# Optimization experiments

Hardware: AMD Instinct MI355X
Metric: run time of the kernel (lower is better)

The kernel has to match this reference:

```python
import jax, jax.numpy as jnp
import numpy as np

N, E, D, F, L = 50000, 250000, 128, 12, 4
EPS_POS = 1e-6
EPS_LN = 1e-5


def setup_inputs() -> dict:
    key = jax.random.key(0)
    ks = iter(jax.random.split(key, 40))
    w = lambda *s: jax.random.normal(next(ks), s, dtype=jnp.float32) * 0.05
    inp = {
        'node_features': jax.random.normal(next(ks), (N, F), dtype=jnp.float32),
        'pos': jax.random.normal(next(ks), (N, 2), dtype=jnp.float32),
        'edge_attr_raw': jax.random.normal(next(ks), (E, F), dtype=jnp.float32),
        'node_proj_w': w(F, D), 'node_proj_b': jnp.zeros((D,), jnp.float32),
        'edge_proj_w': w(F, D), 'edge_proj_b': jnp.zeros((D,), jnp.float32),
        'edge_w1': w(L, 2 * D + 1, D), 'edge_b1': jnp.zeros((L, D), jnp.float32),
        'edge_w2': w(L, D, D), 'edge_b2': jnp.zeros((L, D), jnp.float32),
        'node_w1': w(L, 2 * D, D), 'node_b1': jnp.zeros((L, D), jnp.float32),
        'node_w2': w(L, D, D), 'node_b2': jnp.zeros((L, D), jnp.float32),
        'pos_w1': w(L, D + 1, 1), 'pos_b1': jnp.zeros((L, 1), jnp.float32),
        'pos_w2': w(L, 1, 1), 'pos_b2': jnp.zeros((L, 1), jnp.float32),
        'ln_g': jnp.ones((D,), jnp.float32), 'ln_b': jnp.zeros((D,), jnp.float32),
        'edge_index': jax.random.randint(next(ks), (2, E), 0, N, dtype=jnp.int32),
    }
    return inp


def reference(node_features, pos, edge_attr_raw,
              node_proj_w, node_proj_b, edge_proj_w, edge_proj_b,
              edge_w1, edge_b1, edge_w2, edge_b2,
              node_w1, node_b1, node_w2, node_b2,
              pos_w1, pos_b1, pos_w2, pos_b2,
              ln_g, ln_b, edge_index):
    src, tgt = edge_index[0], edge_index[1]
    n = node_features.shape[0]
    x = node_features @ node_proj_w + node_proj_b          # [N, D]
    # edge_projection output is concatenated then sliced away in the original
    # (edge_input[:, :2D+1]); it is mathematically dead but computed faithfully.
    _edge_attr = edge_attr_raw @ edge_proj_w + edge_proj_b  # dead
    p = pos                                                  # [N, 2]
    for l in range(L):
        xs, xt = x[src], x[tgt]                              # [E, D]
        ps, pt = p[src], p[tgt]                              # [E, 2]
        dist = jnp.linalg.norm(ps - pt, axis=1, keepdims=True)  # [E, 1]
        e_in = jnp.concatenate([xs, xt, dist], axis=1)       # [E, 2D+1]
        msg = jax.nn.silu(e_in @ edge_w1[l] + edge_b1[l]) @ edge_w2[l] + edge_b2[l]
        pos_diff = pt - ps
        pos_unit = pos_diff / (jnp.linalg.norm(pos_diff, axis=1, keepdims=True) + EPS_POS)
        pw = jax.nn.silu(jnp.concatenate([msg, dist], axis=1) @ pos_w1[l] + pos_b1[l])
        pw = pw @ pos_w2[l] + pos_b2[l]                       # [E, 1]
        p = p + jax.ops.segment_sum(pos_unit * pw, tgt, num_segments=n)
        agg = jax.ops.segment_sum(msg, tgt, num_segments=n)  # [N, D]
        n_in = jnp.concatenate([x, agg], axis=1)              # [N, 2D]
        x = x + (jax.nn.silu(n_in @ node_w1[l] + node_b1[l]) @ node_w2[l] + node_b2[l])
    mu = jnp.mean(x, axis=-1, keepdims=True)
    var = jnp.mean(jnp.square(x - mu), axis=-1, keepdims=True)
    x = (x - mu) * jax.lax.rsqrt(var + EPS_LN) * ln_g + ln_b
    return x[None]                                            # [1, N, D]
```

## Files before the change

### kernel.cpp

```cpp
#include <hip/hip_runtime.h>
#include <hip/hip_bf16.h>


#define NNODES 50000
#define NEDGES 250000
#define NTILES 3125
#define MMGRID 512
#define RGRID  1024

typedef unsigned short u16;
typedef __attribute__((ext_vector_type(8))) short bf16x8;
typedef __attribute__((ext_vector_type(4))) float floatx4;

__device__ __forceinline__ float b2f(u16 h){ unsigned u=((unsigned)h)<<16; float f; __builtin_memcpy(&f,&u,4); return f; }
__device__ __forceinline__ u16 f2b(float f){ unsigned u; __builtin_memcpy(&u,&f,4); u = u + 0x7FFFu + ((u>>16)&1u); return (u16)(u>>16); }
__device__ __forceinline__ float siluf(float x){ return x*__builtin_amdgcn_rcpf(1.f+__expf(-x)); }
__device__ __forceinline__ float ldf(const void* p, long i, int isbf){
  return isbf ? b2f(((const u16*)p)[i]) : ((const float*)p)[i];
}

__global__ void detect_kernel(const void* lng, int* flag){
  if (threadIdx.x==0 && blockIdx.x==0) *flag = (((const u16*)lng)[0] != 0) ? 1 : 0;
}

#define SU_W12   192
#define SU_EBW   704
#define SU_W2P   708
#define SU_PPARM 712
#define SU_PROJ  713
#define SU_CVTP  25713
#define SU_END   26104
__global__ __launch_bounds__(256) void setup_kernel(
    const void* __restrict__ ew1, const void* __restrict__ ew2,
    const void* __restrict__ nw1, const void* __restrict__ nw2,
    u16* __restrict__ packed,
    const void* __restrict__ eb2, const void* __restrict__ pw1,
    const void* __restrict__ pb1, const void* __restrict__ pw2v, const void* __restrict__ pb2,
    float* __restrict__ w2p, float* __restrict__ c2p, float* __restrict__ pparm,
    float* __restrict__ ebW,
    const void* __restrict__ nf, const void* __restrict__ npw, const void* __restrict__ npb,
    u16* __restrict__ xb,
    const void* __restrict__ pos, float* __restrict__ pf,
    const int* __restrict__ flagp)
{
  const int isbf = *flagp;
  const int b = blockIdx.x, tid = threadIdx.x;
  __shared__ float red[128];
  if (b < SU_W12){
    int t = b*256 + tid;
    int m = t >> 11; int r = t & 2047;
    int lane = r & 63; int ntk = r >> 6;
    int kk = ntk >> 3, nt = ntk & 7;
    int l = m/6, w = m%6;
    const void* src; long off;
    switch(w){
      case 0: src=ew1; off=(long)l*257*128;            break;
      case 1: src=ew1; off=(long)l*257*128 + 128*128;  break;
      case 2: src=ew2; off=(long)l*128*128;            break;
      case 3: src=nw1; off=(long)l*256*128;            break;
      case 4: src=nw1; off=(long)l*256*128 + 128*128;  break;
      default:src=nw2; off=(long)l*128*128;            break;
    }
    int c  = nt*16 + (lane & 15);
    int k0 = kk*32 + (lane >> 4)*8;
    u16 vals[8];
#pragma unroll
    for (int j=0;j<8;j++){
      long idx = off + (long)(k0+j)*128 + c;
      vals[j] = isbf ? ((const u16*)src)[idx] : f2b(((const float*)src)[idx]);
    }
    bf16x8 v; __builtin_memcpy(&v, vals, 16);
    *(bf16x8*)(packed + (long)t*8) = v;
  } else if (b < SU_EBW){
    int bb = b - SU_W12;
    int l = bb >> 7, k = bb & 127;
    if (tid < 128){
      int j = tid;
      long e2 = (long)l*16384 + (long)k*128;
      long nb = (long)l*256*128 + 128*128;
      float acc = 0.f;
      for (int d=0; d<128; d++)
        acc += ldf(ew2, e2 + d, isbf) * ldf(nw1, nb + (long)d*128 + j, isbf);
      int kk = k>>5, lane = ((k>>3)&3)*16 + (j&15), nt = j>>4, jj = k&7;
      packed[(long)(24+l)*16384 + (long)((kk*8+nt)*64 + lane)*8 + jj] = f2b(acc);
    }
  } else if (b < SU_W2P){
    int l = b - SU_EBW;
    if (tid < 128){
      int j = tid;
      long nb = (long)l*256*128 + 128*128;
      float acc = 0.f;
      for (int d=0; d<128; d++)
        acc += ldf(eb2, (long)l*128 + d, isbf) * ldf(nw1, nb + (long)d*128 + j, isbf);
      ebW[l*128+j] = acc;
    }
  } else if (b < SU_PPARM){
    int l = b - SU_W2P;
    int i = tid;
    long Woff = (long)l*128*128, poff = (long)l*129;
    if (i < 128){
      float acc = 0.f;
      for (int j=0;j<128;j++) acc += ldf(ew2, Woff + (long)i*128 + j, isbf) * ldf(pw1, poff + j, isbf);
      w2p[l*128+i] = acc;
      red[i] = ldf(eb2, (long)l*128 + i, isbf) * ldf(pw1, poff + i, isbf);
    }
    __syncthreads();
    for (int st=64; st>0; st>>=1){ if (i<st) red[i]+=red[i+st]; __syncthreads(); }
    if (i==0) c2p[l] = red[0];
  } else if (b == SU_PPARM){
    int l = tid;
    if (l < 4){
      pparm[l*4+0] = ldf(pw1, (long)l*129 + 128, isbf);
      pparm[l*4+1] = ldf(pb1, l, isbf);
      pparm[l*4+2] = ldf(pw2v, l, isbf);
      pparm[l*4+3] = ldf(pb2, l, isbf);
    }
  } else if (b < SU_CVTP){
    int n = (b - SU_PROJ)*2 + (tid>>7), d = tid & 127;
    if (n < NNODES){
      float acc = ldf(npb, d, isbf);
#pragma unroll
      for (int f=0; f<12; f++) acc += ldf(nf, (long)n*12+f, isbf) * ldf(npw, f*128+d, isbf);
      xb[(long)n*128+d] = f2b(acc);
    }
  } else {
    int i = (b - SU_CVTP)*256 + tid;
    if (i < 2*NNODES) pf[i] = ldf(pos, i, isbf);
  }
}

__global__ __launch_bounds__(256) void hist_kernel(const int* __restrict__ tgt, int* __restrict__ cnt, int E){
  int i = blockIdx.x*256 + threadIdx.x;
  if (i < E) atomicAdd(&cnt[tgt[i]], 1);
}

__global__ __launch_bounds__(256) void bsum_kernel(const int* __restrict__ cnt, int* __restrict__ bsum, int N){
  int i = blockIdx.x*256 + threadIdx.x;
  int v = (i < N) ? cnt[i] : 0;
#pragma unroll
  for (int off=32; off; off>>=1) v += __shfl_down(v, off);
  __shared__ int ws[4];
  if ((threadIdx.x & 63) == 0) ws[threadIdx.x>>6] = v;
  __syncthreads();
  if (threadIdx.x == 0) bsum[blockIdx.x] = ws[0]+ws[1]+ws[2]+ws[3];
}

__global__ __launch_bounds__(256) void bscan_kernel(int* __restrict__ bsum, int nb){
  __shared__ int lds[256];
  int i = threadIdx.x;
  int v = (i < nb) ? bsum[i] : 0;
  lds[i] = v; __syncthreads();
#pragma unroll
  for (int off=1; off<256; off<<=1){
    int t = (i>=off)? lds[i-off] : 0; __syncthreads();
    lds[i] += t; __syncthreads();
  }
  if (i < nb) bsum[i] = lds[i] - v;
}

__global__ __launch_bounds__(256) void csr_kernel(
    const int* __restrict__ cnt, const int* __restrict__ bsum,
    int* __restrict__ rowptr, int* __restrict__ cursor, float* __restrict__ degf, int N)
{
  __shared__ int lds[256];
  int i = blockIdx.x*256 + threadIdx.x;
  int c = (i < N) ? cnt[i] : 0;
  lds[threadIdx.x] = c; __syncthreads();
#pragma unroll
  for (int off=1; off<256; off<<=1){
    int t = (threadIdx.x>=off)? lds[threadIdx.x-off] : 0; __syncthreads();
    lds[threadIdx.x] += t; __syncthreads();
  }
  int run = bsum[blockIdx.x] + lds[threadIdx.x] - c;
  if (i < N){
    rowptr[i] = run; cursor[i] = run; degf[i] = (float)c;
    if (i == N-1) rowptr[N] = run + c;
  }
}

__global__ __launch_bounds__(256) void scatter_kernel(
    const int* __restrict__ src, const int* __restrict__ tgt,
    int* __restrict__ cursor, int* __restrict__ permsrc, int E)
{
  int e = blockIdx.x*256 + threadIdx.x;
  if (e >= E) return;
  int t = tgt[e];
  int p = atomicAdd(&cursor[t], 1);
  permsrc[p] = src[e];
}

__global__ __launch_bounds__(256) void mm_ab_kernel(
    const u16* __restrict__ X, const u16* __restrict__ Wa, const u16* __restrict__ Wb,
    const void* __restrict__ bias, long bias_off,
    u16* __restrict__ Ab, u16* __restrict__ Bb, const int* __restrict__ flagp)
{
  extern __shared__ u16 wlds[];
  const int tid = threadIdx.x, wave = tid>>6, lane = tid&63;
  const int isbf = *flagp;
  const int lr = lane&15, lg = lane>>4;
  for (int i=tid; i<2048; i+=256){
    *(bf16x8*)(wlds + (long)i*8)          = *(const bf16x8*)(Wa + (long)i*8);
    *(bf16x8*)(wlds + 16384 + (long)i*8)  = *(const bf16x8*)(Wb + (long)i*8);
  }
  float biasv[8];
#pragma unroll
  for (int nt=0;nt<8;nt++) biasv[nt] = ldf(bias, bias_off + nt*16 + lr, isbf);
  __syncthreads();
  for (int tile = blockIdx.x*4 + wave; tile < NTILES; tile += MMGRID*4){
    const u16* xr = X + ((long)tile*16 + lr)*128;
    bf16x8 a[4];
#pragma unroll
    for (int kk=0;kk<4;kk++) a[kk] = *(const bf16x8*)(xr + kk*32 + lg*8);
    floatx4 accA[8], accB[8];
#pragma unroll
    for (int i=0;i<8;i++){ accA[i]=(floatx4){0,0,0,0}; accB[i]=(floatx4){0,0,0,0}; }
#pragma unroll
    for (int kk=0;kk<4;kk++){
#pragma unroll
      for (int nt=0;nt<8;nt++){
        bf16x8 ba = *(const bf16x8*)(wlds + ((kk*8+nt)*64 + lane)*8);
        accA[nt] = __builtin_amdgcn_mfma_f32_16x16x32_bf16(a[kk], ba, accA[nt], 0, 0, 0);
        bf16x8 bb = *(const bf16x8*)(wlds + 16384 + ((kk*8+nt)*64 + lane)*8);
        accB[nt] = __builtin_amdgcn_mfma_f32_16x16x32_bf16(a[kk], bb, accB[nt], 0, 0, 0);
      }
    }
#pragma unroll
    for (int r=0;r<4;r++){
      long row = (long)tile*16 + lg*4 + r;
#pragma unroll
      for (int nt=0;nt<8;nt++){
        int col = nt*16 + lr;
        Ab[row*128+col] = f2b(accA[nt][r] + biasv[nt]);
        Bb[row*128+col] = f2b(accB[nt][r]);
      }
    }
  }
}

__global__ __launch_bounds__(256) void mm_hidden_kernel(
    const u16* __restrict__ X, const u16* __restrict__ H,
    const u16* __restrict__ W1, const u16* __restrict__ W2,
    const void* __restrict__ nb1, long nb1_off,
    const float* __restrict__ degf, const float* __restrict__ ebW,
    u16* __restrict__ hb, const int* __restrict__ flagp)
{
  extern __shared__ u16 wlds[];
  const int tid = threadIdx.x, wave = tid>>6, lane = tid&63;
  const int isbf = *flagp;
  const int lr = lane&15, lg = lane>>4;
  for (int i=tid; i<2048; i+=256){
    *(bf16x8*)(wlds + (long)i*8)          = *(const bf16x8*)(W1 + (long)i*8);
    *(bf16x8*)(wlds + 16384 + (long)i*8)  = *(const bf16x8*)(W2 + (long)i*8);
  }
  float nb1v[8], ebv[8];
#pragma unroll
  for (int nt=0;nt<8;nt++){ int col=nt*16+lr; nb1v[nt]=ldf(nb1, nb1_off+col, isbf); ebv[nt]=ebW[col]; }
  __syncthreads();
  for (int tile = blockIdx.x*4 + wave; tile < NTILES; tile += MMGRID*4){
    const u16* xr = X + ((long)tile*16 + lr)*128;
    const u16* hr = H + ((long)tile*16 + lr)*128;
    bf16x8 ax[4], ah[4];
#pragma unroll
    for (int kk=0;kk<4;kk++){
      ax[kk] = *(const bf16x8*)(xr + kk*32 + lg*8);
      ah[kk] = *(const bf16x8*)(hr + kk*32 + lg*8);
    }
    floatx4 acc[8];
#pragma unroll
    for (int i=0;i<8;i++) acc[i]=(floatx4){0,0,0,0};
#pragma unroll
    for (int kk=0;kk<4;kk++){
#pragma unroll
      for (int nt=0;nt<8;nt++){
        bf16x8 b1 = *(const bf16x8*)(wlds + ((kk*8+nt)*64 + lane)*8);
        acc[nt] = __builtin_amdgcn_mfma_f32_16x16x32_bf16(ax[kk], b1, acc[nt], 0, 0, 0);
        bf16x8 b2 = *(const bf16x8*)(wlds + 16384 + ((kk*8+nt)*64 + lane)*8);
        acc[nt] = __builtin_amdgcn_mfma_f32_16x16x32_bf16(ah[kk], b2, acc[nt], 0, 0, 0);
      }
    }
    float dv[4];
#pragma unroll
    for (int r=0;r<4;r++) dv[r] = degf[(long)tile*16 + lg*4 + r];
#pragma unroll
    for (int r=0;r<4;r++){
      long row = (long)tile*16 + lg*4 + r;
#pragma unroll
      for (int nt=0;nt<8;nt++){
        int col = nt*16 + lr;
        hb[row*128+col] = f2b(siluf(acc[nt][r] + nb1v[nt] + dv[r]*ebv[nt]));
      }
    }
  }
}

template<int LN>
__global__ __launch_bounds__(256) void mm_res_kernel(
    const u16* __restrict__ H, const u16* __restrict__ W,
    const void* __restrict__ nb2, long nb2_off,
    u16* __restrict__ xb,
    const void* __restrict__ lng, const void* __restrict__ lnb, void* __restrict__ outp,
    const int* __restrict__ flagp)
{
  extern __shared__ u16 wlds[];
  const int tid = threadIdx.x, wave = tid>>6, lane = tid&63;
  const int isbf = *flagp;
  const int lr = lane&15, lg = lane>>4;
  for (int i=tid; i<2048; i+=256)
    *(bf16x8*)(wlds + (long)i*8) = *(const bf16x8*)(W + (long)i*8);
  float nb2v[8];
#pragma unroll
  for (int nt=0;nt<8;nt++) nb2v[nt] = ldf(nb2, nb2_off + nt*16 + lr, isbf);
  float gv[8], bvv[8];
  if (LN){
#pragma unroll
    for (int nt=0;nt<8;nt++){ int col=nt*16+lr; gv[nt]=ldf(lng,col,isbf); bvv[nt]=ldf(lnb,col,isbf); }
  }
  __syncthreads();
  for (int tile = blockIdx.x*4 + wave; tile < NTILES; tile += RGRID*4){
    const u16* hr = H + ((long)tile*16 + lr)*128;
    bf16x8 a[4];
#pragma unroll
    for (int kk=0;kk<4;kk++) a[kk] = *(const bf16x8*)(hr + kk*32 + lg*8);
    floatx4 acc[8];
#pragma unroll
    for (int i=0;i<8;i++) acc[i]=(floatx4){0,0,0,0};
#pragma unroll
    for (int kk=0;kk<4;kk++){
#pragma unroll
      for (int nt=0;nt<8;nt++){
        bf16x8 b = *(const bf16x8*)(wlds + ((kk*8+nt)*64 + lane)*8);
        acc[nt] = __builtin_amdgcn_mfma_f32_16x16x32_bf16(a[kk], b, acc[nt], 0, 0, 0);
      }
    }
#pragma unroll
    for (int r=0;r<4;r++){
      long row = (long)tile*16 + lg*4 + r;
#pragma unroll
      for (int nt=0;nt<8;nt++){
        int col = nt*16 + lr;
        float v = acc[nt][r] + nb2v[nt] + b2f(xb[row*128+col]);
        acc[nt][r] = v;
        if (!LN) xb[row*128+col] = f2b(v);
      }
    }
    if (LN){
      float s[4] = {0,0,0,0}, q[4] = {0,0,0,0};
#pragma unroll
      for (int r=0;r<4;r++){
#pragma unroll
        for (int nt=0;nt<8;nt++){ float v = acc[nt][r]; s[r] += v; q[r] += v*v; }
      }
#pragma unroll
      for (int mask=1; mask<16; mask<<=1){
#pragma unroll
        for (int r=0;r<4;r++){ s[r] += __shfl_xor(s[r], mask); q[r] += __shfl_xor(q[r], mask); }
      }
#pragma unroll
      for (int r=0;r<4;r++){
        long row = (long)tile*16 + lg*4 + r;
        float mu = s[r]*(1.f/128.f);
        float var = q[r]*(1.f/128.f) - mu*mu;
        float inv = rsqrtf(var + 1e-5f);
#pragma unroll
        for (int nt=0;nt<8;nt++){
          int col = nt*16 + lr;
          float y = (acc[nt][r]-mu)*inv*gv[nt] + bvv[nt];
          if (isbf) ((u16*)outp)[row*128+col] = f2b(y);
          else      ((float*)outp)[row*128+col] = y;
        }
      }
    }
  }
}

__global__ __launch_bounds__(256) void agg_kernel(
    const int* __restrict__ rowptr, const int* __restrict__ permsrc,
    const float* __restrict__ pf_in,
    const u16* __restrict__ A, const u16* __restrict__ B,
    const void* __restrict__ ew1, long w1c_off,
    const float* __restrict__ w2p, const float* __restrict__ c2pl,
    const float* __restrict__ pp,
    u16* __restrict__ Hb, float* __restrict__ pf_out, int N,
    const int* __restrict__ flagp)
{
  const int isbf = *flagp;
  int tid = threadIdx.x, lane = tid & 63;
  int t = blockIdx.x*4 + (tid>>6);
  if (t >= N) return;
  int tu = __builtin_amdgcn_readfirstlane(t);
  float c0 = ldf(ew1, w1c_off + 2*lane,     isbf);
  float c1 = ldf(ew1, w1c_off + 2*lane + 1, isbf);
  float2 wp = *(const float2*)(w2p + 2*lane);
  float c2 = c2pl[0];
  float p0 = pp[0], p1 = pp[1], p2 = pp[2], p3 = pp[3];
  int jb = rowptr[tu], je = rowptr[tu+1];
  float2 pt = *(const float2*)(pf_in + 2*(long)tu);
  unsigned bv = *(const unsigned*)(B + (long)tu*128 + 2*lane);
  float b0 = b2f((u16)bv), b1 = b2f((u16)(bv>>16));
  float h0a = 0.f, h1a = 0.f, dpx = 0.f, dpy = 0.f;
  for (int j0 = jb; j0 < je; j0 += 4){
    int m = je - j0; if (m > 4) m = 4;
    int s[4]; float2 ps[4]; unsigned av[4];
    float part[4], dist[4], dxv[4], dyv[4];
#pragma unroll
    for (int c=0;c<4;c++) if (c<m) s[c] = permsrc[j0+c];
#pragma unroll
    for (int c=0;c<4;c++) if (c<m){
      ps[c] = *(const float2*)(pf_in + 2*(long)s[c]);
      av[c] = *(const unsigned*)(A + (long)s[c]*128 + 2*lane);
    }
#pragma unroll
    for (int c=0;c<4;c++){
      if (c<m){
        float dx = pt.x - ps[c].x, dy = pt.y - ps[c].y;
        float d2 = dx*dx + dy*dy;
        float dd = __builtin_amdgcn_sqrtf(d2);
        float h0 = siluf(b2f((u16)av[c])       + b0 + dd*c0);
        float h1 = siluf(b2f((u16)(av[c]>>16)) + b1 + dd*c1);
        h0a += h0; h1a += h1;
        part[c] = h0*wp.x + h1*wp.y;
        dist[c] = dd; dxv[c] = dx; dyv[c] = dy;
      } else part[c] = 0.f;
    }
#pragma unroll
    for (int off=32; off; off>>=1){
#pragma unroll
      for (int c=0;c<4;c++) part[c] += __shfl_xor(part[c], off);
    }
#pragma unroll
    for (int c=0;c<4;c++){
      if (c<m){
        float spre = part[c] + c2 + dist[c]*p0 + p1;
        float pwv  = siluf(spre)*p2 + p3;
        float inv  = __builtin_amdgcn_rcpf(dist[c] + 1e-6f);
        dpx += dxv[c]*inv*pwv; dpy += dyv[c]*inv*pwv;
      }
    }
  }
  *(unsigned*)(Hb + (long)tu*128 + 2*lane) = (unsigned)f2b(h0a) | ((unsigned)f2b(h1a)<<16);
  if (lane == 0){
    float2 o; o.x = pt.x + dpx; o.y = pt.y + dpy;
    *(float2*)(pf_out + 2*(long)tu) = o;
  }
}

extern "C" void kernel_launch(void* const* d_in, const int* in_sizes, int n_in,
                              void* d_out, int out_size, void* d_ws, size_t ws_size,
                              hipStream_t stream)
{
  const void* nf  = d_in[0];
  const void* pos = d_in[1];
  const void* npw = d_in[3];
  const void* npb = d_in[4];
  const void* ew1 = d_in[7];
  const void* eb1 = d_in[8];
  const void* ew2 = d_in[9];
  const void* eb2 = d_in[10];
  const void* nw1 = d_in[11];
  const void* nb1 = d_in[12];
  const void* nw2 = d_in[13];
  const void* nb2 = d_in[14];
  const void* pw1 = d_in[15];
  const void* pb1 = d_in[16];
  const void* pw2 = d_in[17];
  const void* pb2 = d_in[18];
  const void* lng = d_in[19];
  const void* lnb = d_in[20];
  const int* eidx = (const int*)d_in[21];
  const int N = NNODES, E = NEDGES;
  const int* srcp = eidx;
  const int* tgtp = eidx + E;

  char* w = (char*)d_ws;
  size_t off = 0;
  auto alloc = [&](size_t bytes)->char* { char* p = w + off; off += (bytes + 255)/256*256; return p; };
  u16*   xb    = (u16*)  alloc((size_t)N*128*2);
  u16*   Ab    = (u16*)  alloc((size_t)N*128*2);
  u16*   Bb    = (u16*)  alloc((size_t)N*128*2);
  u16*   Hb    = (u16*)  alloc((size_t)N*128*2);
  float* pf0   = (float*)alloc((size_t)N*2*4);
  float* pf1   = (float*)alloc((size_t)N*2*4);
  int*   cnt   = (int*)  alloc((size_t)N*4);
  int*   rowptr= (int*)  alloc((size_t)(N+1)*4);
  int*   cursor= (int*)  alloc((size_t)N*4);
  float* degf  = (float*)alloc((size_t)N*4);
  int*   perm  = (int*)  alloc((size_t)E*4);
  int*   bsum  = (int*)  alloc(256*4);
  u16*   pk    = (u16*)  alloc((size_t)28*16384*2);
  float* ebW   = (float*)alloc(4*128*4);
  float* w2p   = (float*)alloc(4*128*4);
  float* c2p   = (float*)alloc(4*4);
  float* pparm = (float*)alloc(16*4);
  int*   flag  = (int*)  alloc(4);
  u16* hb = Ab;

  const int NB = (N + 255)/256;
  detect_kernel<<<1, 64, 0, stream>>>(lng, flag);
  hipMemsetAsync(cnt, 0, (size_t)N*4, stream);
  hist_kernel<<<(E+255)/256, 256, 0, stream>>>(tgtp, cnt, E);
  bsum_kernel<<<NB, 256, 0, stream>>>(cnt, bsum, N);
  bscan_kernel<<<1, 256, 0, stream>>>(bsum, NB);
  csr_kernel<<<NB, 256, 0, stream>>>(cnt, bsum, rowptr, cursor, degf, N);
  scatter_kernel<<<(E+255)/256, 256, 0, stream>>>(srcp, tgtp, cursor, perm, E);
  setup_kernel<<<SU_END, 256, 0, stream>>>(
      ew1, ew2, nw1, nw2, pk,
      eb2, pw1, pb1, pw2, pb2,
      w2p, c2p, pparm, ebW,
      nf, npw, npb, xb,
      pos, pf0, flag);

  mm_ab_kernel<<<MMGRID, 256, 65536, stream>>>(xb, pk + 0*16384, pk + 1*16384,
                                               eb1, 0, Ab, Bb, flag);
  for (int l = 0; l < 4; l++){
    const u16* NW1a = pk + (l*6+3)*16384;
    const u16* NW2p = pk + (l*6+5)*16384;
    const u16* W12p = pk + (24+l)*16384;
    float* pin  = (l & 1) ? pf1 : pf0;
    float* pout = (l & 1) ? pf0 : pf1;

    agg_kernel<<<(N+3)/4, 256, 0, stream>>>(
        rowptr, perm, pin, Ab, Bb,
        ew1, (long)l*257*128 + 256*128,
        w2p + l*128, c2p + l, pparm + l*4,
        Hb, pout, N, flag);
    mm_hidden_kernel<<<MMGRID, 256, 65536, stream>>>(
        xb, Hb, NW1a, W12p, nb1, (long)l*128, degf, ebW + l*128, hb, flag);
    if (l < 3){
      mm_res_kernel<0><<<RGRID, 256, 32768, stream>>>(
          hb, NW2p, nb2, (long)l*128, xb, nullptr, nullptr, nullptr, flag);
      mm_ab_kernel<<<MMGRID, 256, 65536, stream>>>(
          xb, pk + ((l+1)*6+0)*16384, pk + ((l+1)*6+1)*16384,
          eb1, (long)(l+1)*128, Ab, Bb, flag);
    } else {
      mm_res_kernel<1><<<RGRID, 256, 32768, stream>>>(
          hb, NW2p, nb2, (long)l*128, xb, lng, lnb, d_out, flag);
    }
  }
}
```

Measured before the change: 524.4 us.

## Merge setup and CSR-build kernels into one cooperative grid-synced kernel

Replaces the detect, memset, histogram, block-sum, scan, CSR, scatter and setup kernels with a single cooperative kernel. It runs these as phases separated by grid.sync and interleaves independent weight-packing work into the phases. The aim is to remove several launch gaps and small-kernel tails. In exchange it adds grid-wide barriers, and a 512-block grid must stride over large phases such as the 25000-block node projection, which may run with lower parallelism than before.

```diff
diff --git a/kernel.cpp b/kernel.cpp
--- a/kernel.cpp
+++ b/kernel.cpp
@@ -1,5 +1,8 @@
 #include <hip/hip_runtime.h>
 #include <hip/hip_bf16.h>
+#include <hip/hip_cooperative_groups.h>
+
+namespace cg = cooperative_groups;
 
 
 #define NNODES 50000
@@ -7,6 +10,7 @@
 #define NTILES 3125
 #define MMGRID 512
 #define RGRID  1024
+#define COOPGRID 512
 
 typedef unsigned short u16;
 typedef __attribute__((ext_vector_type(8))) short bf16x8;
@@ -19,18 +23,22 @@
   return isbf ? b2f(((const u16*)p)[i]) : ((const float*)p)[i];
 }
 
-__global__ void detect_kernel(const void* lng, int* flag){
-  if (threadIdx.x==0 && blockIdx.x==0) *flag = (((const u16*)lng)[0] != 0) ? 1 : 0;
-}
-
-#define SU_W12   192
-#define SU_EBW   704
-#define SU_W2P   708
-#define SU_PPARM 712
-#define SU_PROJ  713
-#define SU_CVTP  25713
-#define SU_END   26104
-__global__ __launch_bounds__(256) void setup_kernel(
+#define P0_MEMSET 196
+#define P0_CVTP   587
+#define P0_END    596
+#define P1_HIST   977
+#define P1_END    1169
+#define P2_BSUM   196
+#define P2_END    708
+#define P3_END    25001
+#define P4_END    196
+#define P5_END    977
+
+__global__ __launch_bounds__(256, 4) void coop_setup_kernel(
+    const void* __restrict__ lng, int* __restrict__ flag,
+    const int* __restrict__ src, const int* __restrict__ tgt,
+    int* __restrict__ cnt, int* __restrict__ bsum, int* __restrict__ rowptr,
+    int* __restrict__ cursor, float* __restrict__ degf, int* __restrict__ permsrc,
     const void* __restrict__ ew1, const void* __restrict__ ew2,
     const void* __restrict__ nw1, const void* __restrict__ nw2,
     u16* __restrict__ packed,
@@ -40,153 +48,169 @@
     float* __restrict__ ebW,
     const void* __restrict__ nf, const void* __restrict__ npw, const void* __restrict__ npb,
     u16* __restrict__ xb,
-    const void* __restrict__ pos, float* __restrict__ pf,
-    const int* __restrict__ flagp)
+    const void* __restrict__ pos, float* __restrict__ pf)
 {
-  const int isbf = *flagp;
-  const int b = blockIdx.x, tid = threadIdx.x;
+  cg::grid_group grid = cg::this_grid();
+  const int tid = threadIdx.x;
+  const int isbf = (((const u16*)lng)[0] != 0) ? 1 : 0;
+  __shared__ int slds[256];
   __shared__ float red[128];
-  if (b < SU_W12){
-    int t = b*256 + tid;
-    int m = t >> 11; int r = t & 2047;
-    int lane = r & 63; int ntk = r >> 6;
-    int kk = ntk >> 3, nt = ntk & 7;
-    int l = m/6, w = m%6;
-    const void* src; long off;
-    switch(w){
-      case 0: src=ew1; off=(long)l*257*128;            break;
-      case 1: src=ew1; off=(long)l*257*128 + 128*128;  break;
-      case 2: src=ew2; off=(long)l*128*128;            break;
-      case 3: src=nw1; off=(long)l*256*128;            break;
-      case 4: src=nw1; off=(long)l*256*128 + 128*128;  break;
-      default:src=nw2; off=(long)l*128*128;            break;
-    }
-    int c  = nt*16 + (lane & 15);
-    int k0 = kk*32 + (lane >> 4)*8;
-    u16 vals[8];
-#pragma unroll
-    for (int j=0;j<8;j++){
-      long idx = off + (long)(k0+j)*128 + c;
-      vals[j] = isbf ? ((const u16*)src)[idx] : f2b(((const float*)src)[idx]);
-    }
-    bf16x8 v; __builtin_memcpy(&v, vals, 16);
-    *(bf16x8*)(packed + (long)t*8) = v;
-  } else if (b < SU_EBW){
-    int bb = b - SU_W12;
-    int l = bb >> 7, k = bb & 127;
-    if (tid < 128){
-      int j = tid;
-      long e2 = (long)l*16384 + (long)k*128;
-      long nb = (long)l*256*128 + 128*128;
-      float acc = 0.f;
-      for (int d=0; d<128; d++)
-        acc += ldf(ew2, e2 + d, isbf) * ldf(nw1, nb + (long)d*128 + j, isbf);
-      int kk = k>>5, lane = ((k>>3)&3)*16 + (j&15), nt = j>>4, jj = k&7;
-      packed[(long)(24+l)*16384 + (long)((kk*8+nt)*64 + lane)*8 + jj] = f2b(acc);
-    }
-  } else if (b < SU_W2P){
-    int l = b - SU_EBW;
-    if (tid < 128){
-      int j = tid;
-      long nb = (long)l*256*128 + 128*128;
-      float acc = 0.f;
-      for (int d=0; d<128; d++)
-        acc += ldf(eb2, (long)l*128 + d, isbf) * ldf(nw1, nb + (long)d*128 + j, isbf);
-      ebW[l*128+j] = acc;
-    }
-  } else if (b < SU_PPARM){
-    int l = b - SU_W2P;
-    int i = tid;
-    long Woff = (long)l*128*128, poff = (long)l*129;
-    if (i < 128){
-      float acc = 0.f;
-      for (int j=0;j<128;j++) acc += ldf(ew2, Woff + (long)i*128 + j, isbf) * ldf(pw1, poff + j, isbf);
-      w2p[l*128+i] = acc;
-      red[i] = ldf(eb2, (long)l*128 + i, isbf) * ldf(pw1, poff + i, isbf);
+  __shared__ int ws4[4];
+  if (blockIdx.x == 0 && tid == 0) *flag = isbf;
+
+  for (int vb = blockIdx.x; vb < P0_END; vb += gridDim.x){
+    if (vb < P0_MEMSET){
+      int i = vb*256 + tid;
+      if (i < NNODES) cnt[i] = 0;
+    } else if (vb < P0_CVTP){
+      int i = (vb - P0_MEMSET)*256 + tid;
+      if (i < 2*NNODES) pf[i] = ldf(pos, i, isbf);
+    } else if (vb == P0_CVTP){
+      if (tid < 4){
+        int l = tid;
+        pparm[l*4+0] = ldf(pw1, (long)l*129 + 128, isbf);
+        pparm[l*4+1] = ldf(pb1, l, isbf);
+        pparm[l*4+2] = ldf(pw2v, l, isbf);
+        pparm[l*4+3] = ldf(pb2, l, isbf);
+      }
+    } else if (vb < P0_CVTP + 5){
+      int l = vb - (P0_CVTP + 1);
+      int i = tid;
+      long Woff = (long)l*128*128, poff = (long)l*129;
+      if (i < 128){
+        float acc = 0.f;
+        for (int j=0;j<128;j++) acc += ldf(ew2, Woff + (long)i*128 + j, isbf) * ldf(pw1, poff + j, isbf);
+        w2p[l*128+i] = acc;
+        red[i] = ldf(eb2, (long)l*128 + i, isbf) * ldf(pw1, poff + i, isbf);
+      }
+      __syncthreads();
+      for (int st=64; st>0; st>>=1){ if (i<st) red[i]+=red[i+st]; __syncthreads(); }
+      if (i==0) c2p[l] = red[0];
+      __syncthreads();
+    } else {
+      int l = vb - (P0_CVTP + 5);
+      if (tid < 128){
+        int j = tid;
+        long nb = (long)l*256*128 + 128*128;
+        float acc = 0.f;
+        for (int d=0; d<128; d++)
+          acc += ldf(eb2, (long)l*128 + d, isbf) * ldf(nw1, nb + (long)d*128 + j, isbf);
+        ebW[l*128+j] = acc;
+      }
+    }
+  }
+  grid.sync();
+
+  for (int vb = blockIdx.x; vb < P1_END; vb += gridDim.x){
+    if (vb < P1_HIST){
+      int i = vb*256 + tid;
+      if (i < NEDGES) atomicAdd(&cnt[tgt[i]], 1);
+    } else {
+      int t = (vb - P1_HIST)*256 + tid;
+      int m = t >> 11; int r = t & 2047;
+      int lane = r & 63; int ntk = r >> 6;
+      int kk = ntk >> 3, nt = ntk & 7;
+      int l = m/6, w = m%6;
+      const void* sp; long off;
+      switch(w){
+        case 0: sp=ew1; off=(long)l*257*128;            break;
+        case 1: sp=ew1; off=(long)l*257*128 + 128*128;  break;
+        case 2: sp=ew2; off=(long)l*128*128;            break;
+        case 3: sp=nw1; off=(long)l*256*128;            break;
+        case 4: sp=nw1; off=(long)l*256*128 + 128*128;  break;
+        default:sp=nw2; off=(long)l*128*128;            break;
+      }
+      int c  = nt*16 + (lane & 15);
+      int k0 = kk*32 + (lane >> 4)*8;
+      u16 vals[8];
+#pragma unroll
+      for (int j=0;j<8;j++){
+        long idx = off + (long)(k0+j)*128 + c;
+        vals[j] = isbf ? ((const u16*)sp)[idx] : f2b(((const float*)sp)[idx]);
+      }
+      bf16x8 v; __builtin_memcpy(&v, vals, 16);
+      *(bf16x8*)(packed + (long)t*8) = v;
+    }
+  }
+  grid.sync();
+
+  for (int vb = blockIdx.x; vb < P2_END; vb += gridDim.x){
+    if (vb < P2_BSUM){
+      int i = vb*256 + tid;
+      int v = (i < NNODES) ? cnt[i] : 0;
+#pragma unroll
+      for (int off=32; off; off>>=1) v += __shfl_down(v, off);
+      if ((tid & 63) == 0) ws4[tid>>6] = v;
+      __syncthreads();
+      if (tid == 0) bsum[vb] = ws4[0]+ws4[1]+ws4[2]+ws4[3];
+      __syncthreads();
+    } else {
+      int bb = vb - P2_BSUM;
+      int l = bb >> 7, k = bb & 127;
+      if (tid < 128){
+        int j = tid;
+        long e2 = (long)l*16384 + (long)k*128;
+        long nb = (long)l*256*128 + 128*128;
+        float acc = 0.f;
+        for (int d=0; d<128; d++)
+          acc += ldf(ew2, e2 + d, isbf) * ldf(nw1, nb + (long)d*128 + j, isbf);
+        int kk = k>>5, lane = ((k>>3)&3)*16 + (j&15), nt = j>>4, jj = k&7;
+        packed[(long)(24+l)*16384 + (long)((kk*8+nt)*64 + lane)*8 + jj] = f2b(acc);
+      }
+    }
+  }
+  grid.sync();
+
+  for (int vb = blockIdx.x; vb < P3_END; vb += gridDim.x){
+    if (vb == 0){
+      int i = tid;
+      int v = (i < 196) ? bsum[i] : 0;
+      slds[i] = v; __syncthreads();
+#pragma unroll
+      for (int off=1; off<256; off<<=1){
+        int t2 = (i>=off)? slds[i-off] : 0; __syncthreads();
+        slds[i] += t2; __syncthreads();
+      }
+      if (i < 196) bsum[i] = slds[i] - v;
+    } else {
+      int nblk = vb - 1;
+      int n = nblk*2 + (tid>>7), d = tid & 127;
+      if (n < NNODES){
+        float acc = ldf(npb, d, isbf);
+#pragma unroll
+        for (int f=0; f<12; f++) acc += ldf(nf, (long)n*12+f, isbf) * ldf(npw, f*128+d, isbf);
+        xb[(long)n*128+d] = f2b(acc);
+      }
+    }
+  }
+  grid.sync();
+
+  for (int vb = blockIdx.x; vb < P4_END; vb += gridDim.x){
+    int i = vb*256 + tid;
+    int c = (i < NNODES) ? cnt[i] : 0;
+    slds[tid] = c; __syncthreads();
+#pragma unroll
+    for (int off=1; off<256; off<<=1){
+      int t2 = (tid>=off)? slds[tid-off] : 0; __syncthreads();
+      slds[tid] += t2; __syncthreads();
+    }
+    int run = bsum[vb] + slds[tid] - c;
+    if (i < NNODES){
+      rowptr[i] = run; cursor[i] = run; degf[i] = (float)c;
+      if (i == NNODES-1) rowptr[NNODES] = run + c;
     }
     __syncthreads();
-    for (int st=64; st>0; st>>=1){ if (i<st) red[i]+=red[i+st]; __syncthreads(); }
-    if (i==0) c2p[l] = red[0];
-  } else if (b == SU_PPARM){
-    int l = tid;
-    if (l < 4){
-      pparm[l*4+0] = ldf(pw1, (long)l*129 + 128, isbf);
-      pparm[l*4+1] = ldf(pb1, l, isbf);
-      pparm[l*4+2] = ldf(pw2v, l, isbf);
-      pparm[l*4+3] = ldf(pb2, l, isbf);
-    }
-  } else if (b < SU_CVTP){
-    int n = (b - SU_PROJ)*2 + (tid>>7), d = tid & 127;
-    if (n < NNODES){
-      float acc = ldf(npb, d, isbf);
-#pragma unroll
-      for (int f=0; f<12; f++) acc += ldf(nf, (long)n*12+f, isbf) * ldf(npw, f*128+d, isbf);
-      xb[(long)n*128+d] = f2b(acc);
-    }
-  } else {
-    int i = (b - SU_CVTP)*256 + tid;
-    if (i < 2*NNODES) pf[i] = ldf(pos, i, isbf);
-  }
-}
-
-__global__ __launch_bounds__(256) void hist_kernel(const int* __restrict__ tgt, int* __restrict__ cnt, int E){
-  int i = blockIdx.x*256 + threadIdx.x;
-  if (i < E) atomicAdd(&cnt[tgt[i]], 1);
-}
-
-__global__ __launch_bounds__(256) void bsum_kernel(const int* __restrict__ cnt, int* __restrict__ bsum, int N){
-  int i = blockIdx.x*256 + threadIdx.x;
-  int v = (i < N) ? cnt[i] : 0;
-#pragma unroll
-  for (int off=32; off; off>>=1) v += __shfl_down(v, off);
-  __shared__ int ws[4];
-  if ((threadIdx.x & 63) == 0) ws[threadIdx.x>>6] = v;
-  __syncthreads();
-  if (threadIdx.x == 0) bsum[blockIdx.x] = ws[0]+ws[1]+ws[2]+ws[3];
-}
-
-__global__ __launch_bounds__(256) void bscan_kernel(int* __restrict__ bsum, int nb){
-  __shared__ int lds[256];
-  int i = threadIdx.x;
-  int v = (i < nb) ? bsum[i] : 0;
-  lds[i] = v; __syncthreads();
-#pragma unroll
-  for (int off=1; off<256; off<<=1){
-    int t = (i>=off)? lds[i-off] : 0; __syncthreads();
-    lds[i] += t; __syncthreads();
-  }
-  if (i < nb) bsum[i] = lds[i] - v;
-}
-
-__global__ __launch_bounds__(256) void csr_kernel(
-    const int* __restrict__ cnt, const int* __restrict__ bsum,
-    int* __restrict__ rowptr, int* __restrict__ cursor, float* __restrict__ degf, int N)
-{
-  __shared__ int lds[256];
-  int i = blockIdx.x*256 + threadIdx.x;
-  int c = (i < N) ? cnt[i] : 0;
-  lds[threadIdx.x] = c; __syncthreads();
-#pragma unroll
-  for (int off=1; off<256; off<<=1){
-    int t = (threadIdx.x>=off)? lds[threadIdx.x-off] : 0; __syncthreads();
-    lds[threadIdx.x] += t; __syncthreads();
-  }
-  int run = bsum[blockIdx.x] + lds[threadIdx.x] - c;
-  if (i < N){
-    rowptr[i] = run; cursor[i] = run; degf[i] = (float)c;
-    if (i == N-1) rowptr[N] = run + c;
-  }
-}
-
-__global__ __launch_bounds__(256) void scatter_kernel(
-    const int* __restrict__ src, const int* __restrict__ tgt,
-    int* __restrict__ cursor, int* __restrict__ permsrc, int E)
-{
-  int e = blockIdx.x*256 + threadIdx.x;
-  if (e >= E) return;
-  int t = tgt[e];
-  int p = atomicAdd(&cursor[t], 1);
-  permsrc[p] = src[e];
+  }
+  grid.sync();
+
+  for (int vb = blockIdx.x; vb < P5_END; vb += gridDim.x){
+    int e = vb*256 + tid;
+    if (e < NEDGES){
+      int t2 = tgt[e];
+      int p = atomicAdd(&cursor[t2], 1);
+      permsrc[p] = src[e];
+    }
+  }
 }
 
 __global__ __launch_bounds__(256) void mm_ab_kernel(
@@ -494,20 +518,16 @@
   int*   flag  = (int*)  alloc(4);
   u16* hb = Ab;
 
-  const int NB = (N + 255)/256;
-  detect_kernel<<<1, 64, 0, stream>>>(lng, flag);
-  hipMemsetAsync(cnt, 0, (size_t)N*4, stream);
-  hist_kernel<<<(E+255)/256, 256, 0, stream>>>(tgtp, cnt, E);
-  bsum_kernel<<<NB, 256, 0, stream>>>(cnt, bsum, N);
-  bscan_kernel<<<1, 256, 0, stream>>>(bsum, NB);
-  csr_kernel<<<NB, 256, 0, stream>>>(cnt, bsum, rowptr, cursor, degf, N);
-  scatter_kernel<<<(E+255)/256, 256, 0, stream>>>(srcp, tgtp, cursor, perm, E);
-  setup_kernel<<<SU_END, 256, 0, stream>>>(
-      ew1, ew2, nw1, nw2, pk,
-      eb2, pw1, pb1, pw2, pb2,
-      w2p, c2p, pparm, ebW,
-      nf, npw, npb, xb,
-      pos, pf0, flag);
+  void* kargs[] = {
+    (void*)&lng, (void*)&flag, (void*)&srcp, (void*)&tgtp,
+    (void*)&cnt, (void*)&bsum, (void*)&rowptr, (void*)&cursor, (void*)&degf, (void*)&perm,
+    (void*)&ew1, (void*)&ew2, (void*)&nw1, (void*)&nw2, (void*)&pk,
+    (void*)&eb2, (void*)&pw1, (void*)&pb1, (void*)&pw2, (void*)&pb2,
+    (void*)&w2p, (void*)&c2p, (void*)&pparm, (void*)&ebW,
+    (void*)&nf, (void*)&npw, (void*)&npb, (void*)&xb,
+    (void*)&pos, (void*)&pf0
+  };
+  hipLaunchCooperativeKernel(coop_setup_kernel, dim3(COOPGRID), dim3(256), kargs, 0, stream);
 
   mm_ab_kernel<<<MMGRID, 256, 65536, stream>>>(xb, pk + 0*16384, pk + 1*16384,
                                                eb1, 0, Ab, Bb, flag);
```

Result: slower. 874.3 us (+66.7%).

## Store node feature matrices in MFMA-tile swizzled layout for coalesced stores

Applied to the files above, without the earlier changes.

Node feature buffers (x, A, B, H) switch from row-major to a 16-row tile swizzled layout that matches the MFMA accumulator output, so each matmul epilogue writes contiguous 64-lane runs instead of scattered 2-byte stores. The A-operand loads and the gather in agg_kernel are rewritten to index the new layout, and agg_kernel's block-to-node mapping is permuted to line up with it. The cost is that gathers in agg now touch 16-byte chunks spread across a tile, which may weaken locality for random source rows.

```diff
diff --git a/kernel.cpp b/kernel.cpp
--- a/kernel.cpp
+++ b/kernel.cpp
@@ -17,6 +17,9 @@
 __device__ __forceinline__ float siluf(float x){ return x*__builtin_amdgcn_rcpf(1.f+__expf(-x)); }
 __device__ __forceinline__ float ldf(const void* p, long i, int isbf){
   return isbf ? b2f(((const u16*)p)[i]) : ((const float*)p)[i];
+}
+__device__ __forceinline__ long swz(long row, int col){
+  return (row>>4)*2048 + (long)(((col>>4)*4 + (int)(row&3))*64 + (((int)(row&15))>>2)*16 + (col&15));
 }
 
 __global__ void detect_kernel(const void* lng, int* flag){
@@ -121,7 +124,7 @@
       float acc = ldf(npb, d, isbf);
 #pragma unroll
       for (int f=0; f<12; f++) acc += ldf(nf, (long)n*12+f, isbf) * ldf(npw, f*128+d, isbf);
-      xb[(long)n*128+d] = f2b(acc);
+      xb[swz(n, d)] = f2b(acc);
     }
   } else {
     int i = (b - SU_CVTP)*256 + tid;
@@ -205,12 +208,15 @@
   float biasv[8];
 #pragma unroll
   for (int nt=0;nt<8;nt++) biasv[nt] = ldf(bias, bias_off + nt*16 + lr, isbf);
+  int aoff[4];
+#pragma unroll
+  for (int kk=0;kk<4;kk++) aoff[kk] = ((2*kk + (lg>>1))*4 + (lr&3))*64 + (lr>>2)*16 + (lg&1)*8;
   __syncthreads();
   for (int tile = blockIdx.x*4 + wave; tile < NTILES; tile += MMGRID*4){
-    const u16* xr = X + ((long)tile*16 + lr)*128;
+    const u16* xt = X + (long)tile*2048;
     bf16x8 a[4];
 #pragma unroll
-    for (int kk=0;kk<4;kk++) a[kk] = *(const bf16x8*)(xr + kk*32 + lg*8);
+    for (int kk=0;kk<4;kk++) a[kk] = *(const bf16x8*)(xt + aoff[kk]);
     floatx4 accA[8], accB[8];
 #pragma unroll
     for (int i=0;i<8;i++){ accA[i]=(floatx4){0,0,0,0}; accB[i]=(floatx4){0,0,0,0}; }
@@ -224,14 +230,15 @@
         accB[nt] = __builtin_amdgcn_mfma_f32_16x16x32_bf16(a[kk], bb, accB[nt], 0, 0, 0);
       }
     }
+    u16* at = Ab + (long)tile*2048;
+    u16* bt = Bb + (long)tile*2048;
 #pragma unroll
     for (int r=0;r<4;r++){
-      long row = (long)tile*16 + lg*4 + r;
 #pragma unroll
       for (int nt=0;nt<8;nt++){
-        int col = nt*16 + lr;
-        Ab[row*128+col] = f2b(accA[nt][r] + biasv[nt]);
-        Bb[row*128+col] = f2b(accB[nt][r]);
+        int o = (nt*4+r)*64 + lane;
+        at[o] = f2b(accA[nt][r] + biasv[nt]);
+        bt[o] = f2b(accB[nt][r]);
       }
     }
   }
@@ -255,15 +262,18 @@
   float nb1v[8], ebv[8];
 #pragma unroll
   for (int nt=0;nt<8;nt++){ int col=nt*16+lr; nb1v[nt]=ldf(nb1, nb1_off+col, isbf); ebv[nt]=ebW[col]; }
+  int aoff[4];
+#pragma unroll
+  for (int kk=0;kk<4;kk++) aoff[kk] = ((2*kk + (lg>>1))*4 + (lr&3))*64 + (lr>>2)*16 + (lg&1)*8;
   __syncthreads();
   for (int tile = blockIdx.x*4 + wave; tile < NTILES; tile += MMGRID*4){
-    const u16* xr = X + ((long)tile*16 + lr)*128;
-    const u16* hr = H + ((long)tile*16 + lr)*128;
+    const u16* xt = X + (long)tile*2048;
+    const u16* ht = H + (long)tile*2048;
     bf16x8 ax[4], ah[4];
 #pragma unroll
     for (int kk=0;kk<4;kk++){
-      ax[kk] = *(const bf16x8*)(xr + kk*32 + lg*8);
-      ah[kk] = *(const bf16x8*)(hr + kk*32 + lg*8);
+      ax[kk] = *(const bf16x8*)(xt + aoff[kk]);
+      ah[kk] = *(const bf16x8*)(ht + aoff[kk]);
     }
     floatx4 acc[8];
 #pragma unroll
@@ -281,13 +291,12 @@
     float dv[4];
 #pragma unroll
     for (int r=0;r<4;r++) dv[r] = degf[(long)tile*16 + lg*4 + r];
+    u16* ot = hb + (long)tile*2048;
 #pragma unroll
     for (int r=0;r<4;r++){
-      long row = (long)tile*16 + lg*4 + r;
 #pragma unroll
       for (int nt=0;nt<8;nt++){
-        int col = nt*16 + lr;
-        hb[row*128+col] = f2b(siluf(acc[nt][r] + nb1v[nt] + dv[r]*ebv[nt]));
+        ot[(nt*4+r)*64 + lane] = f2b(siluf(acc[nt][r] + nb1v[nt] + dv[r]*ebv[nt]));
       }
     }
   }
@@ -315,12 +324,15 @@
 #pragma unroll
     for (int nt=0;nt<8;nt++){ int col=nt*16+lr; gv[nt]=ldf(lng,col,isbf); bvv[nt]=ldf(lnb,col,isbf); }
   }
+  int aoff[4];
+#pragma unroll
+  for (int kk=0;kk<4;kk++) aoff[kk] = ((2*kk + (lg>>1))*4 + (lr&3))*64 + (lr>>2)*16 + (lg&1)*8;
   __syncthreads();
   for (int tile = blockIdx.x*4 + wave; tile < NTILES; tile += RGRID*4){
-    const u16* hr = H + ((long)tile*16 + lr)*128;
+    const u16* ht = H + (long)tile*2048;
     bf16x8 a[4];
 #pragma unroll
-    for (int kk=0;kk<4;kk++) a[kk] = *(const bf16x8*)(hr + kk*32 + lg*8);
+    for (int kk=0;kk<4;kk++) a[kk] = *(const bf16x8*)(ht + aoff[kk]);
     floatx4 acc[8];
 #pragma unroll
     for (int i=0;i<8;i++) acc[i]=(floatx4){0,0,0,0};
@@ -332,15 +344,15 @@
         acc[nt] = __builtin_amdgcn_mfma_f32_16x16x32_bf16(a[kk], b, acc[nt], 0, 0, 0);
       }
     }
+    u16* xt = xb + (long)tile*2048;
 #pragma unroll
     for (int r=0;r<4;r++){
-      long row = (long)tile*16 + lg*4 + r;
 #pragma unroll
       for (int nt=0;nt<8;nt++){
-        int col = nt*16 + lr;
-        float v = acc[nt][r] + nb2v[nt] + b2f(xb[row*128+col]);
+        int o = (nt*4+r)*64 + lane;
+        float v = acc[nt][r] + nb2v[nt] + b2f(xt[o]);
         acc[nt][r] = v;
-        if (!LN) xb[row*128+col] = f2b(v);
+        if (!LN) xt[o] = f2b(v);
       }
     }
     if (LN){
@@ -385,9 +397,10 @@
 {
   const int isbf = *flagp;
   int tid = threadIdx.x, lane = tid & 63;
-  int t = blockIdx.x*4 + (tid>>6);
+  int t = ((blockIdx.x>>2)<<4) + (blockIdx.x&3) + ((tid>>6)<<2);
   if (t >= N) return;
   int tu = __builtin_amdgcn_readfirstlane(t);
+  const int csw = ((lane>>3)*4)*64 + 2*(lane&7);
   float c0 = ldf(ew1, w1c_off + 2*lane,     isbf);
   float c1 = ldf(ew1, w1c_off + 2*lane + 1, isbf);
   float2 wp = *(const float2*)(w2p + 2*lane);
@@ -395,7 +408,8 @@
   float p0 = pp[0], p1 = pp[1], p2 = pp[2], p3 = pp[3];
   int jb = rowptr[tu], je = rowptr[tu+1];
   float2 pt = *(const float2*)(pf_in + 2*(long)tu);
-  unsigned bv = *(const unsigned*)(B + (long)tu*128 + 2*lane);
+  long tuo = (long)(tu>>4)*2048 + (tu&3)*64 + ((tu&15)>>2)*16 + csw;
+  unsigned bv = *(const unsigned*)(B + tuo);
   float b0 = b2f((u16)bv), b1 = b2f((u16)(bv>>16));
   float h0a = 0.f, h1a = 0.f, dpx = 0.f, dpy = 0.f;
   for (int j0 = jb; j0 < je; j0 += 4){
@@ -407,7 +421,8 @@
 #pragma unroll
     for (int c=0;c<4;c++) if (c<m){
       ps[c] = *(const float2*)(pf_in + 2*(long)s[c]);
-      av[c] = *(const unsigned*)(A + (long)s[c]*128 + 2*lane);
+      long so = (long)(s[c]>>4)*2048 + (s[c]&3)*64 + ((s[c]&15)>>2)*16 + csw;
+      av[c] = *(const unsigned*)(A + so);
     }
 #pragma unroll
     for (int c=0;c<4;c++){
@@ -437,7 +452,7 @@
       }
     }
   }
-  *(unsigned*)(Hb + (long)tu*128 + 2*lane) = (unsigned)f2b(h0a) | ((unsigned)f2b(h1a)<<16);
+  *(unsigned*)(Hb + tuo) = (unsigned)f2b(h0a) | ((unsigned)f2b(h1a)<<16);
   if (lane == 0){
     float2 o; o.x = pt.x + dpx; o.y = pt.y + dpy;
     *(float2*)(pf_out + 2*(long)tu) = o;
```

New measurement: 563.6 us. 1.07x slower.
